# Optimization experiments

Measured on AMD Instinct MI355X. Metric: run time of the kernel, lower is better.

The kernel has to match this reference:

```python
import jax, jax.numpy as jnp
import numpy as np

N_NODES = 100000

def _gcn_layer(x, src, dst, norm, W, b, num_nodes):
    # GCNConv: linear transform first, then normalized gather-scatter aggregate
    h = x @ W                                   # [N, F_out]
    msgs = h[src] * norm[:, None]               # [E+N, F_out]
    agg = jax.ops.segment_sum(msgs, dst, num_segments=num_nodes)
    return agg + b


def setup_inputs() -> dict:
    key = jax.random.key(0)
    k1, k2, k3, k4 = jax.random.split(key, 4)
    N, E = N_NODES, 3200000
    x = jax.random.normal(k1, (N, 5), dtype=jnp.float32)
    edge_index = jax.random.randint(k2, (2, E), 0, N, dtype=jnp.int32)
    # Glorot-ish init for the two GCN layers
    W1 = jax.random.normal(k3, (5, 16), dtype=jnp.float32) * (1.0 / np.sqrt(5.0))
    b1 = jnp.zeros((16,), dtype=jnp.float32)
    W2 = jax.random.normal(k4, (16, 3), dtype=jnp.float32) * (1.0 / np.sqrt(16.0))
    b2 = jnp.zeros((3,), dtype=jnp.float32)
    return {"x": x, "edge_index": edge_index, "W1": W1, "b1": b1, "W2": W2, "b2": b2}


def reference(x, edge_index, W1, b1, W2, b2):
    N = x.shape[0]
    # Add self-loops (GCNConv default add_self_loops=True)
    loop = jnp.arange(N, dtype=edge_index.dtype)
    src = jnp.concatenate([edge_index[0], loop])
    dst = jnp.concatenate([edge_index[1], loop])
    # Symmetric normalization: deg computed over destination (in-degree incl. self-loop)
    deg = jax.ops.segment_sum(jnp.ones_like(src, dtype=x.dtype), dst, num_segments=N)
    dinv = jnp.where(deg > 0, jax.lax.rsqrt(deg), 0.0)
    norm = dinv[src] * dinv[dst]                # [E+N]

    h = _gcn_layer(x, src, dst, norm, W1, b1, N)
    h = jax.nn.relu(h)
    out = _gcn_layer(h, src, dst, norm, W2, b2, N)
    return out
```

## Files before the change

kernel.cpp:

```cpp
#include <hip/hip_runtime.h>
#include <cmath>


constexpr int BLK   = 256;
constexpr int VPT   = 16;
constexpr int GPAD  = 16;
constexpr int MAXIT = 9;

__global__ void k_init(int* __restrict__ gcurs, int NB, int stride) {
    int i = blockIdx.x * BLK + threadIdx.x;
    if (i < NB) gcurs[i * GPAD] = i * stride;
}

__global__ __launch_bounds__(BLK) void k_bscatter(
        const int* __restrict__ src, const int* __restrict__ dst,
        int* __restrict__ gcurs, int* __restrict__ bpack,
        int E, int NB, int stride) {
    __shared__ int lcnt[512];
    __shared__ int lbase[512];
    int tid = threadIdx.x;
    for (int i = tid; i < 512; i += BLK) lcnt[i] = 0;
    __syncthreads();
    int e0 = blockIdx.x * (BLK * VPT);
    int pk[VPT];
#pragma unroll
    for (int j = 0; j < VPT; ++j) {
        int e = e0 + j * BLK + tid;
        if (e < E) {
            int b = dst[e] >> 8;
            int r = atomicAdd(&lcnt[b], 1);
            pk[j] = (r << 9) | b;
        } else pk[j] = -1;
    }
    __syncthreads();
    for (int i = tid; i < NB; i += BLK) {
        int c = lcnt[i];
        lbase[i] = c ? atomicAdd(&gcurs[i * GPAD], c) : 0;
    }
    __syncthreads();
#pragma unroll
    for (int j = 0; j < VPT; ++j) {
        if (pk[j] >= 0) {
            int e = e0 + j * BLK + tid;
            int b = pk[j] & 511, r = pk[j] >> 9;
            int p = lbase[b] + r;
            if (p < (b + 1) * stride)
                bpack[p] = (src[e] << 8) | (dst[e] & 255);
        }
    }
}

__global__ __launch_bounds__(1024) void k_sortdeg(
        const int* __restrict__ gcurs, const int* __restrict__ bpack,
        const float* __restrict__ x, float* __restrict__ dinv,
        float* __restrict__ xd8, int* __restrict__ ssrc,
        int* __restrict__ nstart, int N, int stride) {
    __shared__ int cnt[256];
    __shared__ int scan[256];
    int tid = threadIdx.x, b = blockIdx.x;
    if (tid < 256) cnt[tid] = 0;
    __syncthreads();
    int beg = b * stride;
    int end = min(gcurs[b * GPAD], beg + stride);
    int rk[MAXIT], pkv[MAXIT];
#pragma unroll
    for (int j = 0; j < MAXIT; ++j) {
        int e = beg + j * 1024 + tid;
        bool v = e < end;
        int pk = v ? bpack[e] : 0;
        pkv[j] = pk;
        rk[j] = v ? atomicAdd(&cnt[pk & 255], 1) : 0;
    }
    __syncthreads();
    if (tid < 256) scan[tid] = cnt[tid];
    __syncthreads();
    for (int off = 1; off < 256; off <<= 1) {
        int v = 0;
        if (tid < 256 && tid >= off) v = scan[tid - off];
        __syncthreads();
        if (tid < 256) scan[tid] += v;
        __syncthreads();
    }
#pragma unroll
    for (int j = 0; j < MAXIT; ++j) {
        int e = beg + j * 1024 + tid;
        if (e < end) {
            int d = pkv[j] & 255;
            int p = beg + scan[d] - cnt[d] + rk[j];
            ssrc[p] = pkv[j] >> 8;
        }
    }
    if (tid >= 256) return;
    nstart[b * 256 + tid] = beg + scan[tid] - cnt[tid];
    int node = b * 256 + tid;
    if (node >= N) return;
    float di = rsqrtf((float)(cnt[tid] + 1));
    dinv[node] = di;
    float4 lo, hi;
    lo.x = x[(size_t)node * 5 + 0] * di;
    lo.y = x[(size_t)node * 5 + 1] * di;
    lo.z = x[(size_t)node * 5 + 2] * di;
    lo.w = x[(size_t)node * 5 + 3] * di;
    hi.x = x[(size_t)node * 5 + 4] * di;
    hi.y = 0.f; hi.z = 0.f; hi.w = 0.f;
    float4* o = reinterpret_cast<float4*>(xd8) + (size_t)node * 2;
    o[0] = lo; o[1] = hi;
}

__global__ __launch_bounds__(1024) void k_agg1(
        const float* __restrict__ xd8, const int* __restrict__ gcurs,
        const int* __restrict__ ssrc, const int* __restrict__ nstart,
        const float* __restrict__ dinv, const float* __restrict__ W1,
        const float* __restrict__ b1, const float* __restrict__ W2,
        float* __restrict__ hs2, int N, int stride) {
    __shared__ float w1[80];
    __shared__ float w2[48];
    int tid = threadIdx.x, b = blockIdx.x;
    if (tid < 80) w1[tid] = W1[tid];
    else if (tid >= 128 && tid < 176) w2[tid - 128] = W2[tid - 128];
    __syncthreads();
    int n = tid >> 2, q = tid & 3;
    int node = b * 256 + n;
    int beg = b * stride;
    int bend = min(gcurs[b * GPAD], beg + stride);
    int s0 = nstart[b * 256 + n];
    int s1 = (n < 255) ? nstart[b * 256 + n + 1] : bend;
    const float4* h4 = reinterpret_cast<const float4*>(xd8);
    float g0 = 0.f, g1 = 0.f, g2 = 0.f, g3 = 0.f, g4 = 0.f;
    int e = s0 + q;
    int sN = (e < s1) ? ssrc[e] : 0;
    while (e < s1) {
        int s = sN;
        int e2 = e + 4;
        sN = (e2 < s1) ? ssrc[e2] : 0;
        float4 lo = h4[(size_t)s * 2];
        float v4 = xd8[(size_t)s * 8 + 4];
        g0 += lo.x; g1 += lo.y; g2 += lo.z; g3 += lo.w; g4 += v4;
        e = e2;
    }
    g0 += __shfl_xor(g0, 1); g0 += __shfl_xor(g0, 2);
    g1 += __shfl_xor(g1, 1); g1 += __shfl_xor(g1, 2);
    g2 += __shfl_xor(g2, 1); g2 += __shfl_xor(g2, 2);
    g3 += __shfl_xor(g3, 1); g3 += __shfl_xor(g3, 2);
    g4 += __shfl_xor(g4, 1); g4 += __shfl_xor(g4, 2);
    if (q != 0 || node >= N) return;
    float di = dinv[node];
    const float* xs = &xd8[(size_t)node * 8];
    g0 += xs[0]; g1 += xs[1]; g2 += xs[2]; g3 += xs[3]; g4 += xs[4];
    float p0 = 0.f, p1 = 0.f, p2 = 0.f;
#pragma unroll
    for (int f = 0; f < 16; ++f) {
        float s = g0 * w1[f] + g1 * w1[16 + f] + g2 * w1[32 + f]
                + g3 * w1[48 + f] + g4 * w1[64 + f];
        float t = fmaxf(fmaf(di, s, b1[f]), 0.f);
        p0 = fmaf(t, w2[f * 3 + 0], p0);
        p1 = fmaf(t, w2[f * 3 + 1], p1);
        p2 = fmaf(t, w2[f * 3 + 2], p2);
    }
    float4 o = {p0 * di, p1 * di, p2 * di, 0.f};
    *reinterpret_cast<float4*>(&hs2[(size_t)node * 4]) = o;
}

__global__ __launch_bounds__(1024) void k_agg2(
        const float* __restrict__ hs2, const int* __restrict__ gcurs,
        const int* __restrict__ ssrc, const int* __restrict__ nstart,
        const float* __restrict__ dinv, const float* __restrict__ b2,
        float* __restrict__ out, int N, int stride) {
    int tid = threadIdx.x, b = blockIdx.x;
    int n = tid >> 2, q = tid & 3;
    int node = b * 256 + n;
    int beg = b * stride;
    int bend = min(gcurs[b * GPAD], beg + stride);
    int s0 = nstart[b * 256 + n];
    int s1 = (n < 255) ? nstart[b * 256 + n + 1] : bend;
    const float4* h4 = reinterpret_cast<const float4*>(hs2);
    float a0 = 0.f, a1 = 0.f, a2 = 0.f;
    int e = s0 + q;
    int sN = (e < s1) ? ssrc[e] : 0;
    while (e < s1) {
        int s = sN;
        int e2 = e + 4;
        sN = (e2 < s1) ? ssrc[e2] : 0;
        float4 v = h4[s];
        a0 += v.x; a1 += v.y; a2 += v.z;
        e = e2;
    }
    a0 += __shfl_xor(a0, 1); a0 += __shfl_xor(a0, 2);
    a1 += __shfl_xor(a1, 1); a1 += __shfl_xor(a1, 2);
    a2 += __shfl_xor(a2, 1); a2 += __shfl_xor(a2, 2);
    if (q != 0 || node >= N) return;
    float di = dinv[node];
    const float* hself = &hs2[(size_t)node * 4];
    out[(size_t)node * 3 + 0] = fmaf(di, a0 + hself[0], b2[0]);
    out[(size_t)node * 3 + 1] = fmaf(di, a1 + hself[1], b2[1]);
    out[(size_t)node * 3 + 2] = fmaf(di, a2 + hself[2], b2[2]);
}


extern "C" void kernel_launch(void* const* d_in, const int* in_sizes, int n_in,
                              void* d_out, int out_size, void* d_ws, size_t ws_size,
                              hipStream_t stream) {
    const float* x  = (const float*)d_in[0];
    const int*   ei = (const int*)  d_in[1];
    const float* W1 = (const float*)d_in[2];
    const float* b1 = (const float*)d_in[3];
    const float* W2 = (const float*)d_in[4];
    const float* b2 = (const float*)d_in[5];
    float* out = (float*)d_out;

    const int N = in_sizes[0] / 5;
    const int E = in_sizes[1] / 2;
    const int* src = ei;
    const int* dst = ei + E;

    const int NB = (N + 255) >> 8;
    int mean = (E + NB - 1) / NB;
    int stride = mean + (int)(8.0 * sqrt((double)mean)) + 64;
    stride = (stride + 63) & ~63;
    if (stride > 1024 * MAXIT) stride = 1024 * MAXIT;

    char* ws = (char*)d_ws;
    size_t off = 0;
    auto alloc = [&](size_t bytes) -> void* {
        void* p = ws + off;
        off += (bytes + 15) & ~size_t(15);
        return p;
    };
    int*   gcurs  = (int*)  alloc((size_t)NB * GPAD * 4);
    int*   bpack  = (int*)  alloc((size_t)NB * stride * 4);
    int*   ssrc   = (int*)  alloc((size_t)NB * stride * 4);
    int*   nstart = (int*)  alloc((size_t)NB * 256 * 4);
    float* dinv   = (float*)alloc((size_t)N * 4);
    float* xd8    = (float*)alloc((size_t)N * 8 * 4);
    float* hs2    = (float*)alloc((size_t)N * 4 * 4);
    (void)ws_size; (void)n_in; (void)out_size;

    const int gInit = (NB + BLK - 1) / BLK;
    const int gScat = (E + BLK * VPT - 1) / (BLK * VPT);

    k_init    <<<gInit, BLK,  0, stream>>>(gcurs, NB, stride);
    k_bscatter<<<gScat, BLK,  0, stream>>>(src, dst, gcurs, bpack, E, NB, stride);
    k_sortdeg <<<NB,    1024, 0, stream>>>(gcurs, bpack, x, dinv, xd8, ssrc, nstart, N, stride);
    k_agg1    <<<NB,    1024, 0, stream>>>(xd8, gcurs, ssrc, nstart, dinv, W1, b1, W2, hs2, N, stride);
    k_agg2    <<<NB,    1024, 0, stream>>>(hs2, gcurs, ssrc, nstart, dinv, b2, out, N, stride);
}
```

Baseline: 213.6 us.

## Shard per-bucket global cursors into eight sub-cursors to cut atomic contention

```diff
diff --git a/kernel.cpp b/kernel.cpp
--- a/kernel.cpp
+++ b/kernel.cpp
@@ -5,20 +5,22 @@
 constexpr int BLK   = 256;
 constexpr int VPT   = 16;
 constexpr int GPAD  = 16;
-constexpr int MAXIT = 9;
-
-__global__ void k_init(int* __restrict__ gcurs, int NB, int stride) {
+constexpr int NSUB  = 8;
+constexpr int MAXIT = 10;
+
+__global__ void k_init(int* __restrict__ gcurs, int NC, int stride, int substride) {
     int i = blockIdx.x * BLK + threadIdx.x;
-    if (i < NB) gcurs[i * GPAD] = i * stride;
+    if (i < NC) gcurs[i * GPAD] = (i >> 3) * stride + (i & 7) * substride;
 }
 
 __global__ __launch_bounds__(BLK) void k_bscatter(
         const int* __restrict__ src, const int* __restrict__ dst,
         int* __restrict__ gcurs, int* __restrict__ bpack,
-        int E, int NB, int stride) {
+        int E, int NB, int stride, int substride) {
     __shared__ int lcnt[512];
     __shared__ int lbase[512];
     int tid = threadIdx.x;
+    int sub = blockIdx.x & (NSUB - 1);
     for (int i = tid; i < 512; i += BLK) lcnt[i] = 0;
     __syncthreads();
     int e0 = blockIdx.x * (BLK * VPT);
@@ -35,7 +37,7 @@
     __syncthreads();
     for (int i = tid; i < NB; i += BLK) {
         int c = lcnt[i];
-        lbase[i] = c ? atomicAdd(&gcurs[i * GPAD], c) : 0;
+        lbase[i] = c ? atomicAdd(&gcurs[(i * NSUB + sub) * GPAD], c) : 0;
     }
     __syncthreads();
 #pragma unroll
@@ -44,7 +46,7 @@
             int e = e0 + j * BLK + tid;
             int b = pk[j] & 511, r = pk[j] >> 9;
             int p = lbase[b] + r;
-            if (p < (b + 1) * stride)
+            if (p < b * stride + (sub + 1) * substride)
                 bpack[p] = (src[e] << 8) | (dst[e] & 255);
         }
     }
@@ -54,19 +56,28 @@
         const int* __restrict__ gcurs, const int* __restrict__ bpack,
         const float* __restrict__ x, float* __restrict__ dinv,
         float* __restrict__ xd8, int* __restrict__ ssrc,
-        int* __restrict__ nstart, int N, int stride) {
+        int* __restrict__ nstart, int N, int stride, int substride, int subrecip) {
     __shared__ int cnt[256];
     __shared__ int scan[256];
+    __shared__ int subend[NSUB];
     int tid = threadIdx.x, b = blockIdx.x;
     if (tid < 256) cnt[tid] = 0;
+    if (tid >= 256 && tid < 256 + NSUB) {
+        int r = tid - 256;
+        int sb = b * stride + r * substride;
+        subend[r] = min(gcurs[(b * NSUB + r) * GPAD], sb + substride);
+    }
     __syncthreads();
     int beg = b * stride;
-    int end = min(gcurs[b * GPAD], beg + stride);
     int rk[MAXIT], pkv[MAXIT];
+    bool va[MAXIT];
 #pragma unroll
     for (int j = 0; j < MAXIT; ++j) {
-        int e = beg + j * 1024 + tid;
-        bool v = e < end;
+        int off = j * 1024 + tid;
+        int r = (off * subrecip) >> 24;
+        int e = beg + off;
+        bool v = (off < NSUB * substride) && (e < subend[r]);
+        va[j] = v;
         int pk = v ? bpack[e] : 0;
         pkv[j] = pk;
         rk[j] = v ? atomicAdd(&cnt[pk & 255], 1) : 0;
@@ -83,15 +94,15 @@
     }
 #pragma unroll
     for (int j = 0; j < MAXIT; ++j) {
-        int e = beg + j * 1024 + tid;
-        if (e < end) {
+        if (va[j]) {
             int d = pkv[j] & 255;
             int p = beg + scan[d] - cnt[d] + rk[j];
             ssrc[p] = pkv[j] >> 8;
         }
     }
     if (tid >= 256) return;
-    nstart[b * 256 + tid] = beg + scan[tid] - cnt[tid];
+    nstart[b * 257 + tid] = beg + scan[tid] - cnt[tid];
+    if (tid == 255) nstart[b * 257 + 256] = beg + scan[255];
     int node = b * 256 + tid;
     if (node >= N) return;
     float di = rsqrtf((float)(cnt[tid] + 1));
@@ -108,11 +119,10 @@
 }
 
 __global__ __launch_bounds__(1024) void k_agg1(
-        const float* __restrict__ xd8, const int* __restrict__ gcurs,
-        const int* __restrict__ ssrc, const int* __restrict__ nstart,
-        const float* __restrict__ dinv, const float* __restrict__ W1,
-        const float* __restrict__ b1, const float* __restrict__ W2,
-        float* __restrict__ hs2, int N, int stride) {
+        const float* __restrict__ xd8, const int* __restrict__ ssrc,
+        const int* __restrict__ nstart, const float* __restrict__ dinv,
+        const float* __restrict__ W1, const float* __restrict__ b1,
+        const float* __restrict__ W2, float* __restrict__ hs2, int N) {
     __shared__ float w1[80];
     __shared__ float w2[48];
     int tid = threadIdx.x, b = blockIdx.x;
@@ -121,10 +131,8 @@
     __syncthreads();
     int n = tid >> 2, q = tid & 3;
     int node = b * 256 + n;
-    int beg = b * stride;
-    int bend = min(gcurs[b * GPAD], beg + stride);
-    int s0 = nstart[b * 256 + n];
-    int s1 = (n < 255) ? nstart[b * 256 + n + 1] : bend;
+    int s0 = nstart[b * 257 + n];
+    int s1 = nstart[b * 257 + n + 1];
     const float4* h4 = reinterpret_cast<const float4*>(xd8);
     float g0 = 0.f, g1 = 0.f, g2 = 0.f, g3 = 0.f, g4 = 0.f;
     int e = s0 + q;
@@ -162,17 +170,14 @@
 }
 
 __global__ __launch_bounds__(1024) void k_agg2(
-        const float* __restrict__ hs2, const int* __restrict__ gcurs,
-        const int* __restrict__ ssrc, const int* __restrict__ nstart,
-        const float* __restrict__ dinv, const float* __restrict__ b2,
-        float* __restrict__ out, int N, int stride) {
+        const float* __restrict__ hs2, const int* __restrict__ ssrc,
+        const int* __restrict__ nstart, const float* __restrict__ dinv,
+        const float* __restrict__ b2, float* __restrict__ out, int N) {
     int tid = threadIdx.x, b = blockIdx.x;
     int n = tid >> 2, q = tid & 3;
     int node = b * 256 + n;
-    int beg = b * stride;
-    int bend = min(gcurs[b * GPAD], beg + stride);
-    int s0 = nstart[b * 256 + n];
-    int s1 = (n < 255) ? nstart[b * 256 + n + 1] : bend;
+    int s0 = nstart[b * 257 + n];
+    int s1 = nstart[b * 257 + n + 1];
     const float4* h4 = reinterpret_cast<const float4*>(hs2);
     float a0 = 0.f, a1 = 0.f, a2 = 0.f;
     int e = s0 + q;
@@ -214,10 +219,12 @@
     const int* dst = ei + E;
 
     const int NB = (N + 255) >> 8;
-    int mean = (E + NB - 1) / NB;
-    int stride = mean + (int)(8.0 * sqrt((double)mean)) + 64;
-    stride = (stride + 63) & ~63;
-    if (stride > 1024 * MAXIT) stride = 1024 * MAXIT;
+    int meanSub = (E + NB * NSUB - 1) / (NB * NSUB);
+    int substride = meanSub + (int)(8.0 * sqrt((double)meanSub)) + 1;
+    substride = (substride + 63) & ~63;
+    if (substride * NSUB > 1024 * MAXIT) substride = (1024 * MAXIT) / NSUB;
+    int stride = substride * NSUB;
+    int subrecip = ((1 << 24) + substride - 1) / substride;
 
     char* ws = (char*)d_ws;
     size_t off = 0;
@@ -226,21 +233,23 @@
         off += (bytes + 15) & ~size_t(15);
         return p;
     };
-    int*   gcurs  = (int*)  alloc((size_t)NB * GPAD * 4);
+    int*   gcurs  = (int*)  alloc((size_t)NB * NSUB * GPAD * 4);
     int*   bpack  = (int*)  alloc((size_t)NB * stride * 4);
     int*   ssrc   = (int*)  alloc((size_t)NB * stride * 4);
-    int*   nstart = (int*)  alloc((size_t)NB * 256 * 4);
+    int*   nstart = (int*)  alloc((size_t)NB * 257 * 4);
     float* dinv   = (float*)alloc((size_t)N * 4);
     float* xd8    = (float*)alloc((size_t)N * 8 * 4);
     float* hs2    = (float*)alloc((size_t)N * 4 * 4);
     (void)ws_size; (void)n_in; (void)out_size;
 
-    const int gInit = (NB + BLK - 1) / BLK;
+    const int NC    = NB * NSUB;
+    const int gInit = (NC + BLK - 1) / BLK;
     const int gScat = (E + BLK * VPT - 1) / (BLK * VPT);
 
-    k_init    <<<gInit, BLK,  0, stream>>>(gcurs, NB, stride);
-    k_bscatter<<<gScat, BLK,  0, stream>>>(src, dst, gcurs, bpack, E, NB, stride);
-    k_sortdeg <<<NB,    1024, 0, stream>>>(gcurs, bpack, x, dinv, xd8, ssrc, nstart, N, stride);
-    k_agg1    <<<NB,    1024, 0, stream>>>(xd8, gcurs, ssrc, nstart, dinv, W1, b1, W2, hs2, N, stride);
-    k_agg2    <<<NB,    1024, 0, stream>>>(hs2, gcurs, ssrc, nstart, dinv, b2, out, N, stride);
-}
+    k_init    <<<gInit, BLK,  0, stream>>>(gcurs, NC, stride, substride);
+    k_bscatter<<<gScat, BLK,  0, stream>>>(src, dst, gcurs, bpack, E, NB, stride, substride);
+    k_sortdeg <<<NB,    1024, 0, stream>>>(gcurs, bpack, x, dinv, xd8, ssrc, nstart,
+                                           N, stride, substride, subrecip);
+    k_agg1    <<<NB,    1024, 0, stream>>>(xd8, ssrc, nstart, dinv, W1, b1, W2, hs2, N);
+    k_agg2    <<<NB,    1024, 0, stream>>>(hs2, ssrc, nstart, dinv, b2, out, N);
+}
```

Result: faster. 195.2 us (-8.6%).
